# Performance work log

Measured on AMD Instinct MI355X. Metric: run time of the kernel, lower is better.

The kernel has to match this reference:

```python
import jax, jax.numpy as jnp
import numpy as np

B, S, D = 2, 2048, 2048
H = 16
HD = D // H  # 128
ROPE_BASE = 10000.0


def _rope_cos_sin(seq_len, head_dim):
    inv_freq = 1.0 / (ROPE_BASE ** (jnp.arange(0, head_dim, 2, dtype=jnp.float32) / head_dim))
    t = jnp.arange(seq_len, dtype=jnp.float32)
    freqs = jnp.einsum('i,j->ij', t, inv_freq)  # [S, HD/2]
    emb = jnp.concatenate([freqs, freqs], axis=-1)  # [S, HD]
    return jnp.cos(emb)[None, None], jnp.sin(emb)[None, None]  # [1,1,S,HD]


def _rotate_half(x):
    x1, x2 = jnp.split(x, 2, axis=-1)
    return jnp.concatenate([-x2, x1], axis=-1)


def setup_inputs() -> dict:
    key = jax.random.key(0)
    k1, k2, k3 = jax.random.split(key, 3)
    hidden_states = jax.random.normal(k1, (B, S, D), dtype=jnp.float32)
    w_qkv = jax.random.normal(k2, (D, 3 * D), dtype=jnp.float32) * (D ** -0.5)
    w_o = jax.random.normal(k3, (D, D), dtype=jnp.float32) * (D ** -0.5)
    return {"hidden_states": hidden_states, "w_qkv": w_qkv, "w_o": w_o}


def reference(hidden_states, w_qkv, w_o):
    b, s, _ = hidden_states.shape
    qkv = jnp.einsum('bsd,de->bse', hidden_states, w_qkv)  # [B,S,3D]
    q, k, v = jnp.split(qkv, 3, axis=-1)
    # [B,H,S,HD]
    q = q.reshape(b, s, H, HD).transpose(0, 2, 1, 3)
    k = k.reshape(b, s, H, HD).transpose(0, 2, 1, 3)
    v = v.reshape(b, s, H, HD).transpose(0, 2, 1, 3)
    cos, sin = _rope_cos_sin(s, HD)
    q = q * cos + _rotate_half(q) * sin
    k = k * cos + _rotate_half(k) * sin
    scale = 1.0 / np.sqrt(HD).astype(np.float32)
    scores = jnp.einsum('bhqd,bhkd->bhqk', q, k) * scale  # [B,H,S,S]
    causal = jnp.triu(jnp.ones((s, s), dtype=bool), k=1)
    scores = jnp.where(causal, -jnp.inf, scores)
    attn = jax.nn.softmax(scores, axis=-1)
    out = jnp.einsum('bhqk,bhkd->bhqd', attn, v)  # [B,H,S,HD]
    out = out.transpose(0, 2, 1, 3).reshape(b, s, H * HD)
    return jnp.einsum('bsd,de->bse', out, w_o)
```

## Files before the change

### kernel.cpp

```cpp
#include <hip/hip_runtime.h>
#include <math.h>

typedef unsigned short u16;
typedef short s16x8 __attribute__((ext_vector_type(8)));
typedef float f32x4 __attribute__((ext_vector_type(4)));

#define ATTN_SCALE 0.08838834764831845f
#define NEG_BIG -1.0e30f

__device__ __forceinline__ u16 f2bf(float f) {
  union { float f; unsigned u; } c; c.f = f;
  return (u16)((c.u + 0x7fffu + ((c.u >> 16) & 1u)) >> 16);
}
__device__ __forceinline__ float bf2f(u16 v) {
  union { unsigned u; float f; } c; c.u = ((unsigned)v) << 16;
  return c.f;
}
__device__ __forceinline__ f32x4 mfma16(s16x8 a, s16x8 b, f32x4 c) {
  return __builtin_amdgcn_mfma_f32_16x16x32_bf16(a, b, c, 0, 0, 0);
}
__device__ __forceinline__ void gl_lds16(const u16* g, u16* l) {
  __builtin_amdgcn_global_load_lds(
      (const __attribute__((address_space(1))) unsigned int*)g,
      (__attribute__((address_space(3))) unsigned int*)l, 16, 0, 0);
}

__global__ __launch_bounds__(256) void k_cast(const float* __restrict__ in,
                                              u16* __restrict__ out, int n4) {
  const int i = blockIdx.x * 256 + threadIdx.x;
  if (i >= n4) return;
  const float4 v = ((const float4*)in)[i];
  ushort4 o;
  o.x = f2bf(v.x); o.y = f2bf(v.y); o.z = f2bf(v.z); o.w = f2bf(v.w);
  ((ushort4*)out)[i] = o;
}

__global__ __launch_bounds__(256) void k_transpose_cast(const float* __restrict__ in,
                                                        u16* __restrict__ out,
                                                        int R, int C) {
  __shared__ __attribute__((aligned(16))) u16 tile[32][33];
  const int c0 = blockIdx.x * 32, r0 = blockIdx.y * 32;
  const int tx = threadIdx.x, ty = threadIdx.y;
#pragma unroll
  for (int i = 0; i < 4; ++i)
    tile[ty + 8 * i][tx] = f2bf(in[(r0 + ty + 8 * i) * C + c0 + tx]);
  __syncthreads();
#pragma unroll
  for (int i = 0; i < 4; ++i)
    out[(c0 + ty + 8 * i) * R + r0 + tx] = tile[tx][ty + 8 * i];
}

__global__ __launch_bounds__(256) void k_vtrans(const u16* __restrict__ qkv,
                                                u16* __restrict__ vt) {
  __shared__ __attribute__((aligned(16))) u16 tile[32][33];
  const int bh = blockIdx.z, b = bh >> 4, h = bh & 15;
  const int s0 = blockIdx.x * 32, d0 = blockIdx.y * 32;
  const int tx = threadIdx.x, ty = threadIdx.y;
#pragma unroll
  for (int i = 0; i < 4; ++i) {
    const int s = s0 + ty + 8 * i;
    tile[ty + 8 * i][tx] = qkv[(b * 2048 + s) * 6144 + 4096 + h * 128 + d0 + tx];
  }
  __syncthreads();
#pragma unroll
  for (int i = 0; i < 4; ++i) {
    const int d = d0 + ty + 8 * i;
    vt[bh * 262144 + d * 2048 + s0 + tx] = tile[tx][ty + 8 * i];
  }
}

__global__ __launch_bounds__(256) void k_rope(u16* __restrict__ qkv) {
  const int id = blockIdx.x * 256 + threadIdx.x;
  const int j = id & 63;
  const int h = (id >> 6) & 15;
  const int sec = (id >> 10) & 1;
  const int m = id >> 11;
  const int s = m & 2047;
  const int base = m * 6144 + sec * 2048 + h * 128 + j;
  const float q0 = bf2f(qkv[base]);
  const float q1 = bf2f(qkv[base + 64]);
  const float inv = exp2f((float)j * -0.20762050593046014f);
  const float ang = (float)s * inv;
  float c, sn;
  sincosf(ang, &sn, &c);
  qkv[base]      = f2bf(q0 * c - q1 * sn);
  qkv[base + 64] = f2bf(q1 * c + q0 * sn);
}

template <bool A_F32, typename OUT_T>
__global__ __launch_bounds__(256) void k_gemm_lds(const void* __restrict__ Ap, int lda,
                                                  const u16* __restrict__ BT,
                                                  OUT_T* __restrict__ C, int ldc,
                                                  int K) {
  __shared__ __attribute__((aligned(16))) u16 As[128 * 32];
  __shared__ __attribute__((aligned(16))) u16 Bs[128 * 32];
  const int tid = threadIdx.x;
  const int lane = tid & 63, wave = tid >> 6;
  const int lm = lane & 15, quad = lane >> 4;
  const int wm = wave >> 1, wn = wave & 1;
  const int m0 = blockIdx.y * 128, n0 = blockIdx.x * 128;
  const int srow = lane >> 2, scol = (lane & 3) * 8;

  const f32x4 fzero = {0.f, 0.f, 0.f, 0.f};
  f32x4 acc[4][4];
#pragma unroll
  for (int i = 0; i < 4; ++i)
#pragma unroll
    for (int j = 0; j < 4; ++j) acc[i][j] = fzero;

  for (int k0 = 0; k0 < K; k0 += 32) {
    __syncthreads();
    if constexpr (A_F32) {
      const float* Af = (const float*)Ap;
#pragma unroll
      for (int i = 0; i < 2; ++i) {
        const int seg = tid + 256 * i;
        const int row = seg >> 2, c8 = (seg & 3) * 8;
        const float4 u = *(const float4*)&Af[(m0 + row) * lda + k0 + c8];
        const float4 w = *(const float4*)&Af[(m0 + row) * lda + k0 + c8 + 4];
        uint4 pk;
        pk.x = (unsigned)f2bf(u.x) | ((unsigned)f2bf(u.y) << 16);
        pk.y = (unsigned)f2bf(u.z) | ((unsigned)f2bf(u.w) << 16);
        pk.z = (unsigned)f2bf(w.x) | ((unsigned)f2bf(w.y) << 16);
        pk.w = (unsigned)f2bf(w.z) | ((unsigned)f2bf(w.w) << 16);
        *(uint4*)&As[row * 32 + c8] = pk;
      }
#pragma unroll
      for (int j = 0; j < 2; ++j) {
        const int rb = wave * 32 + j * 16;
        gl_lds16(&BT[(n0 + rb + srow) * K + k0 + scol], &Bs[rb * 32]);
      }
    } else {
      const u16* Ab = (const u16*)Ap;
#pragma unroll
      for (int j = 0; j < 2; ++j) {
        const int rb = wave * 32 + j * 16;
        gl_lds16(&Ab[(m0 + rb + srow) * lda + k0 + scol], &As[rb * 32]);
        gl_lds16(&BT[(n0 + rb + srow) * K + k0 + scol], &Bs[rb * 32]);
      }
    }
    __syncthreads();

    s16x8 af[4], bfr[4];
#pragma unroll
    for (int t = 0; t < 4; ++t) {
      af[t]  = *(const s16x8*)&As[(wm * 64 + t * 16 + lm) * 32 + quad * 8];
      bfr[t] = *(const s16x8*)&Bs[(wn * 64 + t * 16 + lm) * 32 + quad * 8];
    }
#pragma unroll
    for (int mt = 0; mt < 4; ++mt)
#pragma unroll
      for (int nt = 0; nt < 4; ++nt)
        acc[mt][nt] = mfma16(af[mt], bfr[nt], acc[mt][nt]);
  }
#pragma unroll
  for (int mt = 0; mt < 4; ++mt)
#pragma unroll
    for (int nt = 0; nt < 4; ++nt)
#pragma unroll
      for (int r = 0; r < 4; ++r) {
        const float v = acc[mt][nt][r];
        const int idx = (m0 + wm * 64 + mt * 16 + quad * 4 + r) * ldc +
                        n0 + wn * 64 + nt * 16 + lm;
        if constexpr (sizeof(OUT_T) == 2) C[idx] = f2bf(v);
        else                              C[idx] = v;
      }
}

__global__ __launch_bounds__(256) void k_attn(u16* __restrict__ qkv,
                                              const u16* __restrict__ vt) {
  __shared__ __attribute__((aligned(16))) u16 Ks[64 * 136];
  __shared__ __attribute__((aligned(16))) u16 Vs[128 * 72];
  __shared__ __attribute__((aligned(16))) u16 Ps[4 * 16 * 72];
  const int pair = blockIdx.x, bh = blockIdx.y;
  const int b = bh >> 4, h = bh & 15;
  const int tid = threadIdx.x;
  const int lane = tid & 63, wave = tid >> 6;
  const int lm = lane & 15, quad = lane >> 4;
  const int pbase = wave * 1152;
  const f32x4 fzero = {0.f, 0.f, 0.f, 0.f};

  for (int phase = 0; phase < 2; ++phase) {
    const int qtile = phase ? (31 - pair) : pair;
    const int qb = qtile * 64;
    const int qrow = qb + wave * 16 + lm;
    const int qoff = (b * 2048 + qrow) * 6144 + h * 128;

    s16x8 qfrag[4];
#pragma unroll
    for (int c = 0; c < 4; ++c)
      qfrag[c] = *(const s16x8*)&qkv[qoff + c * 32 + quad * 8];

    f32x4 o[8];
#pragma unroll
    for (int dt = 0; dt < 8; ++dt) o[dt] = fzero;
    float m_run = NEG_BIG, l_run = 0.f;

    for (int kt = 0; kt <= qtile; ++kt) {
      const int kt0 = kt * 64;
      __syncthreads();
#pragma unroll
      for (int i = 0; i < 4; ++i) {
        const int seg = tid + 256 * i;
        {
          const int row = seg >> 4, c8 = (seg & 15) * 8;
          *(uint4*)&Ks[row * 136 + c8] =
              *(const uint4*)&qkv[(b * 2048 + kt0 + row) * 6144 + 2048 + h * 128 + c8];
        }
        {
          const int row = seg >> 3, c8 = (seg & 7) * 8;
          *(uint4*)&Vs[row * 72 + c8] =
              *(const uint4*)&vt[bh * 262144 + row * 2048 + kt0 + c8];
        }
      }
      __syncthreads();

      f32x4 sa[4];
#pragma unroll
      for (int ss = 0; ss < 4; ++ss) sa[ss] = fzero;
#pragma unroll
      for (int ss = 0; ss < 4; ++ss)
#pragma unroll
        for (int c = 0; c < 4; ++c) {
          s16x8 a = *(const s16x8*)&Ks[(ss * 16 + lm) * 136 + c * 32 + quad * 8];
          sa[ss] = mfma16(a, qfrag[c], sa[ss]);
        }

      float p[4][4];
      float vmax = NEG_BIG;
#pragma unroll
      for (int ss = 0; ss < 4; ++ss)
#pragma unroll
        for (int r = 0; r < 4; ++r) {
          const int kg = kt0 + ss * 16 + quad * 4 + r;
          float v = sa[ss][r] * ATTN_SCALE;
          if (kg > qrow) v = NEG_BIG;
          p[ss][r] = v;
          vmax = fmaxf(vmax, v);
        }
      vmax = fmaxf(vmax, __shfl_xor(vmax, 16, 64));
      vmax = fmaxf(vmax, __shfl_xor(vmax, 32, 64));
      const float m_new = fmaxf(m_run, vmax);
      const float alpha = __expf(m_run - m_new);
      float rsum = 0.f;
#pragma unroll
      for (int ss = 0; ss < 4; ++ss)
#pragma unroll
        for (int r = 0; r < 4; ++r) {
          p[ss][r] = __expf(p[ss][r] - m_new);
          rsum += p[ss][r];
        }
      rsum += __shfl_xor(rsum, 16, 64);
      rsum += __shfl_xor(rsum, 32, 64);
      l_run = l_run * alpha + rsum;
      m_run = m_new;
#pragma unroll
      for (int dt = 0; dt < 8; ++dt) o[dt] *= alpha;

#pragma unroll
      for (int ss = 0; ss < 4; ++ss)
#pragma unroll
        for (int r = 0; r < 4; ++r)
          Ps[pbase + lm * 72 + ss * 16 + quad * 4 + r] = f2bf(p[ss][r]);

      const s16x8 pv0 = *(const s16x8*)&Ps[pbase + lm * 72 + quad * 8];
      const s16x8 pv1 = *(const s16x8*)&Ps[pbase + lm * 72 + 32 + quad * 8];

#pragma unroll
      for (int dt = 0; dt < 8; ++dt) {
        s16x8 a0 = *(const s16x8*)&Vs[(dt * 16 + lm) * 72 + quad * 8];
        s16x8 a1 = *(const s16x8*)&Vs[(dt * 16 + lm) * 72 + 32 + quad * 8];
        o[dt] = mfma16(a1, pv1, mfma16(a0, pv0, o[dt]));
      }
    }

    const float inv_l = 1.0f / l_run;
#pragma unroll
    for (int dt = 0; dt < 8; ++dt)
#pragma unroll
      for (int r = 0; r < 4; ++r)
        qkv[qoff + dt * 16 + quad * 4 + r] = f2bf(o[dt][r] * inv_l);
  }
}

extern "C" void kernel_launch(void* const* d_in, const int* in_sizes, int n_in,
                              void* d_out, int out_size, void* d_ws, size_t ws_size,
                              hipStream_t stream) {
  const float* hidden = (const float*)d_in[0];
  const float* w_qkv  = (const float*)d_in[1];
  const float* w_o    = (const float*)d_in[2];
  float* out = (float*)d_out;
  u16* ws = (u16*)d_ws;

  u16* qkv   = ws;
  u16* wqkvT = ws + 25165824;
  u16* vt    = ws + 25165824;
  u16* woT   = ws + 33554432;
  u16* hb    = ws + 37748736;
  const bool fast = ws_size >= (size_t)46137344 * 2;

  dim3 tb(32, 8);
  k_transpose_cast<<<dim3(192, 64), tb, 0, stream>>>(w_qkv, wqkvT, 2048, 6144);
  if (fast) {
    k_cast<<<8192, 256, 0, stream>>>(hidden, hb, 2097152);
    k_gemm_lds<false, u16><<<dim3(48, 32), 256, 0, stream>>>(hb, 2048, wqkvT,
                                                             qkv, 6144, 2048);
  } else {
    k_gemm_lds<true, u16><<<dim3(48, 32), 256, 0, stream>>>(hidden, 2048, wqkvT,
                                                            qkv, 6144, 2048);
  }
  k_rope<<<32768, 256, 0, stream>>>(qkv);
  k_vtrans<<<dim3(64, 4, 32), tb, 0, stream>>>(qkv, vt);
  k_transpose_cast<<<dim3(64, 64), tb, 0, stream>>>(w_o, woT, 2048, 2048);
  k_attn<<<dim3(16, 32), 256, 0, stream>>>(qkv, vt);
  k_gemm_lds<false, float><<<dim3(16, 32), 256, 0, stream>>>(qkv, 6144, woT,
                                                             out, 2048, 2048);
}
```

Measured before the change: 487.7 us.

## Double-buffer K/V tiles in attention and merge both query phases into one loop

The attention kernel now stages K and V tiles in two LDS buffers. The next tile's global loads go into registers while the current tile is computed, then get written to the spare buffer, which removes one barrier per iteration. The two causal query-tile phases are flattened into a single 33-iteration loop, so the prefetch pipeline also runs across the phase boundary. The grid axes are swapped so head index varies fastest. This costs extra LDS and registers and may lower occupancy.

```diff
diff --git a/kernel.cpp b/kernel.cpp
--- a/kernel.cpp
+++ b/kernel.cpp
@@ -169,10 +169,10 @@
 
 __global__ __launch_bounds__(256) void k_attn(u16* __restrict__ qkv,
                                               const u16* __restrict__ vt) {
-  __shared__ __attribute__((aligned(16))) u16 Ks[64 * 136];
-  __shared__ __attribute__((aligned(16))) u16 Vs[128 * 72];
+  __shared__ __attribute__((aligned(16))) u16 Ks[2][64 * 136];
+  __shared__ __attribute__((aligned(16))) u16 Vs[2][128 * 72];
   __shared__ __attribute__((aligned(16))) u16 Ps[4 * 16 * 72];
-  const int pair = blockIdx.x, bh = blockIdx.y;
+  const int bh = blockIdx.x, pair = blockIdx.y;
   const int b = bh >> 4, h = bh & 15;
   const int tid = threadIdx.x;
   const int lane = tid & 63, wave = tid >> 6;
@@ -180,107 +180,153 @@
   const int pbase = wave * 1152;
   const f32x4 fzero = {0.f, 0.f, 0.f, 0.f};
 
-  for (int phase = 0; phase < 2; ++phase) {
-    const int qtile = phase ? (31 - pair) : pair;
-    const int qb = qtile * 64;
-    const int qrow = qb + wave * 16 + lm;
-    const int qoff = (b * 2048 + qrow) * 6144 + h * 128;
-
-    s16x8 qfrag[4];
-#pragma unroll
-    for (int c = 0; c < 4; ++c)
-      qfrag[c] = *(const s16x8*)&qkv[qoff + c * 32 + quad * 8];
-
-    f32x4 o[8];
-#pragma unroll
-    for (int dt = 0; dt < 8; ++dt) o[dt] = fzero;
-    float m_run = NEG_BIG, l_run = 0.f;
-
-    for (int kt = 0; kt <= qtile; ++kt) {
-      const int kt0 = kt * 64;
+  const int phase_end = pair;
+
+  uint4 kr[4], vr[4];
+  auto load_tile = [&](int kt0) {
+#pragma unroll
+    for (int i = 0; i < 4; ++i) {
+      const int seg = tid + 256 * i;
+      {
+        const int row = seg >> 4, c8 = (seg & 15) * 8;
+        kr[i] = *(const uint4*)&qkv[(b * 2048 + kt0 + row) * 6144 + 2048 + h * 128 + c8];
+      }
+      {
+        const int row = seg >> 3, c8 = (seg & 7) * 8;
+        vr[i] = *(const uint4*)&vt[bh * 262144 + row * 2048 + kt0 + c8];
+      }
+    }
+  };
+  auto store_tile = [&](int buf) {
+#pragma unroll
+    for (int i = 0; i < 4; ++i) {
+      const int seg = tid + 256 * i;
+      {
+        const int row = seg >> 4, c8 = (seg & 15) * 8;
+        *(uint4*)&Ks[buf][row * 136 + c8] = kr[i];
+      }
+      {
+        const int row = seg >> 3, c8 = (seg & 7) * 8;
+        *(uint4*)&Vs[buf][row * 72 + c8] = vr[i];
+      }
+    }
+  };
+
+  load_tile(0);
+  store_tile(0);
+
+  int qtile = pair;
+  int qb = qtile * 64;
+  int qrow = qb + wave * 16 + lm;
+  int qoff = (b * 2048 + qrow) * 6144 + h * 128;
+  s16x8 qfrag[4];
+#pragma unroll
+  for (int c = 0; c < 4; ++c)
+    qfrag[c] = *(const s16x8*)&qkv[qoff + c * 32 + quad * 8];
+  f32x4 o[8];
+#pragma unroll
+  for (int dt = 0; dt < 8; ++dt) o[dt] = fzero;
+  float m_run = NEG_BIG, l_run = 0.f;
+
+  __syncthreads();
+
+  for (int it = 0; it < 33; ++it) {
+    const int kt0 = (it <= phase_end ? it : it - phase_end - 1) * 64;
+    const int buf = it & 1;
+
+    if (it < 32) {
+      const int nkt = (it + 1 <= phase_end ? it + 1 : it - phase_end) * 64;
+      load_tile(nkt);
+    }
+
+    f32x4 sa[4];
+#pragma unroll
+    for (int ss = 0; ss < 4; ++ss) sa[ss] = fzero;
+#pragma unroll
+    for (int ss = 0; ss < 4; ++ss)
+#pragma unroll
+      for (int c = 0; c < 4; ++c) {
+        s16x8 a = *(const s16x8*)&Ks[buf][(ss * 16 + lm) * 136 + c * 32 + quad * 8];
+        sa[ss] = mfma16(a, qfrag[c], sa[ss]);
+      }
+
+    float p[4][4];
+    float vmax = NEG_BIG;
+#pragma unroll
+    for (int ss = 0; ss < 4; ++ss)
+#pragma unroll
+      for (int r = 0; r < 4; ++r) {
+        const int kg = kt0 + ss * 16 + quad * 4 + r;
+        float v = sa[ss][r] * ATTN_SCALE;
+        if (kg > qrow) v = NEG_BIG;
+        p[ss][r] = v;
+        vmax = fmaxf(vmax, v);
+      }
+    vmax = fmaxf(vmax, __shfl_xor(vmax, 16, 64));
+    vmax = fmaxf(vmax, __shfl_xor(vmax, 32, 64));
+    const float m_new = fmaxf(m_run, vmax);
+    const float alpha = __expf(m_run - m_new);
+    float rsum = 0.f;
+#pragma unroll
+    for (int ss = 0; ss < 4; ++ss)
+#pragma unroll
+      for (int r = 0; r < 4; ++r) {
+        p[ss][r] = __expf(p[ss][r] - m_new);
+        rsum += p[ss][r];
+      }
+    rsum += __shfl_xor(rsum, 16, 64);
+    rsum += __shfl_xor(rsum, 32, 64);
+    l_run = l_run * alpha + rsum;
+    m_run = m_new;
+#pragma unroll
+    for (int dt = 0; dt < 8; ++dt) o[dt] *= alpha;
+
+#pragma unroll
+    for (int ss = 0; ss < 4; ++ss)
+#pragma unroll
+      for (int r = 0; r < 4; ++r)
+        Ps[pbase + lm * 72 + ss * 16 + quad * 4 + r] = f2bf(p[ss][r]);
+    const s16x8 pv0 = *(const s16x8*)&Ps[pbase + lm * 72 + quad * 8];
+    const s16x8 pv1 = *(const s16x8*)&Ps[pbase + lm * 72 + 32 + quad * 8];
+
+#pragma unroll
+    for (int dt = 0; dt < 8; ++dt) {
+      s16x8 a0 = *(const s16x8*)&Vs[buf][(dt * 16 + lm) * 72 + quad * 8];
+      s16x8 a1 = *(const s16x8*)&Vs[buf][(dt * 16 + lm) * 72 + 32 + quad * 8];
+      o[dt] = mfma16(a1, pv1, mfma16(a0, pv0, o[dt]));
+    }
+
+    if (it == phase_end) {
+      const float inv_l = 1.0f / l_run;
+#pragma unroll
+      for (int dt = 0; dt < 8; ++dt)
+#pragma unroll
+        for (int r = 0; r < 4; ++r)
+          qkv[qoff + dt * 16 + quad * 4 + r] = f2bf(o[dt][r] * inv_l);
+      qtile = 31 - pair;
+      qb = qtile * 64;
+      qrow = qb + wave * 16 + lm;
+      qoff = (b * 2048 + qrow) * 6144 + h * 128;
+#pragma unroll
+      for (int c = 0; c < 4; ++c)
+        qfrag[c] = *(const s16x8*)&qkv[qoff + c * 32 + quad * 8];
+#pragma unroll
+      for (int dt = 0; dt < 8; ++dt) o[dt] = fzero;
+      m_run = NEG_BIG; l_run = 0.f;
+    }
+
+    if (it < 32) {
+      store_tile(buf ^ 1);
       __syncthreads();
-#pragma unroll
-      for (int i = 0; i < 4; ++i) {
-        const int seg = tid + 256 * i;
-        {
-          const int row = seg >> 4, c8 = (seg & 15) * 8;
-          *(uint4*)&Ks[row * 136 + c8] =
-              *(const uint4*)&qkv[(b * 2048 + kt0 + row) * 6144 + 2048 + h * 128 + c8];
-        }
-        {
-          const int row = seg >> 3, c8 = (seg & 7) * 8;
-          *(uint4*)&Vs[row * 72 + c8] =
-              *(const uint4*)&vt[bh * 262144 + row * 2048 + kt0 + c8];
-        }
-      }
-      __syncthreads();
-
-      f32x4 sa[4];
-#pragma unroll
-      for (int ss = 0; ss < 4; ++ss) sa[ss] = fzero;
-#pragma unroll
-      for (int ss = 0; ss < 4; ++ss)
-#pragma unroll
-        for (int c = 0; c < 4; ++c) {
-          s16x8 a = *(const s16x8*)&Ks[(ss * 16 + lm) * 136 + c * 32 + quad * 8];
-          sa[ss] = mfma16(a, qfrag[c], sa[ss]);
-        }
-
-      float p[4][4];
-      float vmax = NEG_BIG;
-#pragma unroll
-      for (int ss = 0; ss < 4; ++ss)
-#pragma unroll
-        for (int r = 0; r < 4; ++r) {
-          const int kg = kt0 + ss * 16 + quad * 4 + r;
-          float v = sa[ss][r] * ATTN_SCALE;
-          if (kg > qrow) v = NEG_BIG;
-          p[ss][r] = v;
-          vmax = fmaxf(vmax, v);
-        }
-      vmax = fmaxf(vmax, __shfl_xor(vmax, 16, 64));
-      vmax = fmaxf(vmax, __shfl_xor(vmax, 32, 64));
-      const float m_new = fmaxf(m_run, vmax);
-      const float alpha = __expf(m_run - m_new);
-      float rsum = 0.f;
-#pragma unroll
-      for (int ss = 0; ss < 4; ++ss)
-#pragma unroll
-        for (int r = 0; r < 4; ++r) {
-          p[ss][r] = __expf(p[ss][r] - m_new);
-          rsum += p[ss][r];
-        }
-      rsum += __shfl_xor(rsum, 16, 64);
-      rsum += __shfl_xor(rsum, 32, 64);
-      l_run = l_run * alpha + rsum;
-      m_run = m_new;
-#pragma unroll
-      for (int dt = 0; dt < 8; ++dt) o[dt] *= alpha;
-
-#pragma unroll
-      for (int ss = 0; ss < 4; ++ss)
-#pragma unroll
-        for (int r = 0; r < 4; ++r)
-          Ps[pbase + lm * 72 + ss * 16 + quad * 4 + r] = f2bf(p[ss][r]);
-
-      const s16x8 pv0 = *(const s16x8*)&Ps[pbase + lm * 72 + quad * 8];
-      const s16x8 pv1 = *(const s16x8*)&Ps[pbase + lm * 72 + 32 + quad * 8];
-
-#pragma unroll
-      for (int dt = 0; dt < 8; ++dt) {
-        s16x8 a0 = *(const s16x8*)&Vs[(dt * 16 + lm) * 72 + quad * 8];
-        s16x8 a1 = *(const s16x8*)&Vs[(dt * 16 + lm) * 72 + 32 + quad * 8];
-        o[dt] = mfma16(a1, pv1, mfma16(a0, pv0, o[dt]));
-      }
-    }
-
-    const float inv_l = 1.0f / l_run;
-#pragma unroll
-    for (int dt = 0; dt < 8; ++dt)
-#pragma unroll
-      for (int r = 0; r < 4; ++r)
-        qkv[qoff + dt * 16 + quad * 4 + r] = f2bf(o[dt][r] * inv_l);
-  }
+    }
+  }
+
+  const float inv_l = 1.0f / l_run;
+#pragma unroll
+  for (int dt = 0; dt < 8; ++dt)
+#pragma unroll
+    for (int r = 0; r < 4; ++r)
+      qkv[qoff + dt * 16 + quad * 4 + r] = f2bf(o[dt][r] * inv_l);
 }
 
 extern "C" void kernel_launch(void* const* d_in, const int* in_sizes, int n_in,
@@ -312,7 +358,7 @@
   k_rope<<<32768, 256, 0, stream>>>(qkv);
   k_vtrans<<<dim3(64, 4, 32), tb, 0, stream>>>(qkv, vt);
   k_transpose_cast<<<dim3(64, 64), tb, 0, stream>>>(w_o, woT, 2048, 2048);
-  k_attn<<<dim3(16, 32), 256, 0, stream>>>(qkv, vt);
+  k_attn<<<dim3(32, 16), 256, 0, stream>>>(qkv, vt);
   k_gemm_lds<false, float><<<dim3(16, 32), 256, 0, stream>>>(qkv, 6144, woT,
                                                              out, 2048, 2048);
 }
```

Result: slower. 518.1 us (+6.2%).
